# Performance work log

Hardware: AMD Instinct MI355X
Metric: run time of the kernel (lower is better)

Reference implementation:

```python
import jax, jax.numpy as jnp
import numpy as np

NUM_ENT = 50000
NUM_REL = 64
NUM_TRI = 400000
DIN = 128
DOUT = 128
DREL = 128
NUM_HEAD = 8
DH = DOUT // NUM_HEAD


def setup_inputs() -> dict:
    key = jax.random.key(0)
    ks = jax.random.split(key, 9)
    emb_ent = jax.random.normal(ks[0], (NUM_ENT, DIN), jnp.float32)
    emb_rel = jax.random.normal(ks[1], (NUM_REL, DREL), jnp.float32)
    heads = jax.random.randint(ks[2], (NUM_TRI,), 0, NUM_ENT)
    rels = jax.random.randint(ks[3], (NUM_TRI,), 0, NUM_REL)
    tails = jax.random.randint(ks[4], (NUM_TRI,), 0, NUM_ENT)
    triplets = jnp.stack([heads, rels, tails], axis=-1)
    # xavier-normal-like init (stored as [in, out]; torch Linear applies x @ W.T)
    Wa = jax.random.normal(ks[5], (2 * DIN + DREL, DOUT), jnp.float32) * (2.0 / (2 * DIN + DREL + DOUT)) ** 0.5
    ba = jnp.zeros((DOUT,), jnp.float32)
    attn_vec = jax.random.normal(ks[6], (1, NUM_HEAD, DH), jnp.float32) * 0.1
    Wg = jax.random.normal(ks[7], (DIN + DREL, DOUT), jnp.float32) * (2.0 / (DIN + DREL + DOUT)) ** 0.5
    bg = jnp.zeros((DOUT,), jnp.float32)
    return {"emb_ent": emb_ent, "emb_rel": emb_rel, "triplets": triplets,
            "Wa": Wa, "ba": ba, "attn_vec": attn_vec, "Wg": Wg, "bg": bg}


def reference(emb_ent, emb_rel, triplets, Wa, ba, attn_vec, Wg, bg):
    num_ent = emb_ent.shape[0]
    n_head, d_hid = attn_vec.shape[1], attn_vec.shape[2]
    head, rel, tail = triplets[:, 0], triplets[:, 1], triplets[:, 2]

    # in-degree of each entity (as attention-softmax denominator for self_rel)
    ent_freq = jax.ops.segment_sum(jnp.ones(tail.shape, jnp.float32), tail,
                                   num_segments=num_ent)[:, None]
    # torch adds 1e-16 to all entries iff any entry is zero
    ent_freq = ent_freq + jnp.where(jnp.any(ent_freq == 0.0), 1e-16, 0.0)

    # mean relation embedding of incoming edges per entity -> self-loop relation
    self_rel = jax.ops.segment_sum(emb_rel[rel], tail, num_segments=num_ent) / ent_freq

    # append self-loops: one per entity
    emb_rels = jnp.concatenate([emb_rel[rel], self_rel], axis=0)       # [E+N, dr]
    ar = jnp.arange(num_ent)
    head_all = jnp.concatenate([head, ar], axis=0)                     # [E+N]
    tail_all = jnp.concatenate([tail, ar], axis=0)                     # [E+N]

    # attention logits per edge per head
    feat_att = jnp.concatenate([emb_ent[tail_all], emb_ent[head_all], emb_rels], axis=-1)
    h = jnp.tanh(feat_att @ Wa + ba).reshape(-1, n_head, d_hid)
    attn_raw = jnp.sum(h * attn_vec, axis=-1, keepdims=True)           # [E+N, H, 1]

    # segment softmax over edges sharing a tail (every segment has a self-loop)
    amax = jax.ops.segment_max(attn_raw, tail_all, num_segments=num_ent)
    attn_val = jnp.exp(attn_raw - amax[tail_all])
    asum = jax.ops.segment_sum(attn_val, tail_all, num_segments=num_ent)
    beta = attn_val / (asum[tail_all] + 1e-16)                         # [E+N, H, 1]

    # message projection and weighted aggregation
    msg = (jnp.concatenate([emb_ent[head_all], emb_rels], axis=-1) @ Wg + bg)
    msg = msg.reshape(-1, n_head, d_hid)
    out = jax.ops.segment_sum(beta * msg, tail_all, num_segments=num_ent)
    return out.reshape(num_ent, -1)
```

## Files before the change

### kernel.cpp

```cpp
#include <hip/hip_runtime.h>
#include <math.h>

#define NUM_ENT  50000
#define NUM_REL  64
#define NUM_TRI  400000
#define DIN      128
#define CAP      64

#define PACK_BLOCKS  24
#define SMALL_BLOCKS 64
#define ZERO_BLOCKS  196
#define PREP_BLOCKS  (PACK_BLOCKS + SMALL_BLOCKS + ZERO_BLOCKS)

#define ENT_BLOCKS   782
#define SCAT_BLOCKS  391
#define MID_BLOCKS   (ENT_BLOCKS + SCAT_BLOCKS)

typedef __attribute__((ext_vector_type(8))) short bf16x8;
typedef __attribute__((ext_vector_type(4))) float f32x4;

__device__ __forceinline__ float4 f4add(float4 a, float4 b) {
    return make_float4(a.x + b.x, a.y + b.y, a.z + b.z, a.w + b.w);
}

__device__ __forceinline__ unsigned short f2bf(float f) {
    unsigned u = __float_as_uint(f);
    unsigned r = ((u >> 16) & 1u) + 0x7fffu;
    return (unsigned short)((u + r) >> 16);
}
__device__ __forceinline__ float bf2f(unsigned short h) {
    return __uint_as_float(((unsigned)h) << 16);
}
__device__ __forceinline__ float4 ldbf4(const unsigned short* p) {
    ushort4 u = *(const ushort4*)p;
    return make_float4(bf2f(u.x), bf2f(u.y), bf2f(u.z), bf2f(u.w));
}
__device__ __forceinline__ void ldbf8(const unsigned short* p, float4* lo, float4* hi) {
    ushort4 u0 = *(const ushort4*)p;
    ushort4 u1 = *(const ushort4*)(p + 4);
    *lo = make_float4(bf2f(u0.x), bf2f(u0.y), bf2f(u0.z), bf2f(u0.w));
    *hi = make_float4(bf2f(u1.x), bf2f(u1.y), bf2f(u1.z), bf2f(u1.w));
}

__device__ __forceinline__ float tanhf_fast(float x) {
    float e = __expf(2.f * x);
    return 1.f - 2.f * __builtin_amdgcn_rcpf(e + 1.f);
}
__device__ __forceinline__ float tanh_dot4(float4 x, float4 av) {
    return tanhf_fast(x.x) * av.x + tanhf_fast(x.y) * av.y +
           tanhf_fast(x.z) * av.z + tanhf_fast(x.w) * av.w;
}

__global__ __launch_bounds__(256) void k_prep(const float* __restrict__ emb_rel,
                                              const float* __restrict__ Wa,
                                              const float* __restrict__ Wg,
                                              unsigned short* __restrict__ Bpack,
                                              unsigned short* __restrict__ TaTg,
                                              int* __restrict__ deg) {
    __shared__ float s[DIN];
    int b = blockIdx.x;
    int tid = threadIdx.x;

    if (b < PACK_BLOCKS) {
        for (int i = 0; i < 8; i++) {
            int idx = b * 2048 + i * 256 + tid;
            int j    = idx & 7;
            int lane = (idx >> 3) & 63;
            int ks   = (idx >> 9) & 3;
            int t    = (idx >> 11) & 7;
            int w    = idx >> 14;
            int k = ks * 32 + ((lane >> 4) << 3) + j;
            int n = t * 16 + (lane & 15);
            const float* W = (w == 0) ? Wa : (w == 1) ? (Wa + 128 * DIN) : Wg;
            Bpack[idx] = f2bf(W[k * DIN + n]);
        }
    } else if (b < PACK_BLOCKS + SMALL_BLOCKS) {
        int row = b - PACK_BLOCKS;
        if (tid < DIN) s[tid] = emb_rel[row * DIN + tid];
        __syncthreads();
        int j = tid & 127;
        const float* W = (tid < 128) ? (Wa + 256 * DIN) : (Wg + 128 * DIN);
        float acc = 0.f;
#pragma unroll 8
        for (int k = 0; k < DIN; k++) acc += s[k] * W[k * DIN + j];
        int pos = row * 256 + 8 * (j >> 2) + (j & 3) + ((tid < 128) ? 0 : 4);
        TaTg[pos] = f2bf(acc);
    } else {
        int idx = (b - PACK_BLOCKS - SMALL_BLOCKS) * 256 + tid;
        if (idx < NUM_ENT) deg[idx] = 0;
    }
}

__global__ __launch_bounds__(256) void k_mid(const float* __restrict__ X,
                                             const unsigned short* __restrict__ Bpack,
                                             const int* __restrict__ trip,
                                             const float* __restrict__ ba,
                                             const float* __restrict__ bg,
                                             unsigned short* __restrict__ Pt,
                                             unsigned short* __restrict__ PhGh,
                                             int* __restrict__ deg,
                                             int* __restrict__ elist) {
    __shared__ unsigned short As[64][136];
    int b = blockIdx.x;
    int tid = threadIdx.x;

    if (b < ENT_BLOCKS) {
        int m0 = b * 64;
        for (int i = 0; i < 8; i++) {
            int v = tid + i * 256;
            int row = v >> 5;
            int c4 = v & 31;
            int gr = m0 + row;
            if (gr >= NUM_ENT) gr = NUM_ENT - 1;
            float4 x = *(const float4*)&X[gr * DIN + c4 * 4];
            ushort4 h;
            h.x = f2bf(x.x); h.y = f2bf(x.y); h.z = f2bf(x.z); h.w = f2bf(x.w);
            *(ushort4*)&As[row][c4 * 4] = h;
        }
        __syncthreads();

        int w = tid >> 6;
        int q = tid & 63;
        int quad = q >> 4;
        int lrow = w * 16 + (q & 15);
        int gr = m0 + lrow;

        bf16x8 a[4];
#pragma unroll
        for (int ks = 0; ks < 4; ks++)
            a[ks] = *(const bf16x8*)&As[lrow][ks * 32 + quad * 8];

        const bf16x8* Bp = (const bf16x8*)Bpack;
#pragma unroll
        for (int s = 0; s < 3; s++) {
            f32x4 acc[8];
#pragma unroll
            for (int t = 0; t < 8; t++) acc[t] = (f32x4){0.f, 0.f, 0.f, 0.f};
#pragma unroll
            for (int ks = 0; ks < 4; ks++) {
#pragma unroll
                for (int t = 0; t < 8; t++) {
                    bf16x8 wf = Bp[((s * 8 + t) * 4 + ks) * 64 + q];
                    acc[t] = __builtin_amdgcn_mfma_f32_16x16x32_bf16(wf, a[ks], acc[t], 0, 0, 0);
                }
            }
            if (gr < NUM_ENT) {
#pragma unroll
                for (int t = 0; t < 8; t++) {
                    int n0 = t * 16 + quad * 4;
                    float4 bb = make_float4(0.f, 0.f, 0.f, 0.f);
                    if (s == 0) bb = *(const float4*)&ba[n0];
                    if (s == 2) bb = *(const float4*)&bg[n0];
                    ushort4 o;
                    o.x = f2bf(acc[t][0] + bb.x);
                    o.y = f2bf(acc[t][1] + bb.y);
                    o.z = f2bf(acc[t][2] + bb.z);
                    o.w = f2bf(acc[t][3] + bb.w);
                    if (s == 0) {
                        *(ushort4*)&Pt[gr * DIN + n0] = o;
                    } else {
                        *(ushort4*)&PhGh[gr * 256 + 2 * n0 + ((s == 1) ? 0 : 4)] = o;
                    }
                }
            }
        }
    } else {
        int i0 = (b - ENT_BLOCKS) * 1024 + tid * 4;
        if (i0 < NUM_TRI) {
            const int4* tp = (const int4*)&trip[i0 * 3];
            int4 A = tp[0], B4 = tp[1], C4 = tp[2];
            int hs[4] = {A.x, A.w, B4.z, C4.y};
            int rs[4] = {A.y, B4.x, B4.w, C4.z};
            int ts[4] = {A.z, B4.y, C4.x, C4.w};
#pragma unroll
            for (int u = 0; u < 4; u++) {
                int pos = atomicAdd(&deg[ts[u]], 1);
                if (pos < CAP) elist[ts[u] * CAP + pos] = (hs[u] << 6) | rs[u];
            }
        }
    }
}

__global__ __launch_bounds__(256) void k_fused(const int* __restrict__ elist,
                                               const int* __restrict__ deg_arr,
                                               const unsigned short* __restrict__ Pt,
                                               const unsigned short* __restrict__ PhGh,
                                               const unsigned short* __restrict__ TaTg,
                                               const float* __restrict__ attn_vec,
                                               float* __restrict__ out) {
    int tid = threadIdx.x;
    int wv = tid >> 6;
    int lane = tid & 63;
    int half = lane >> 5;
    int q = lane & 31;
    int t = blockIdx.x * 4 + wv;
    int deg = deg_arr[t];
    if (deg > CAP) deg = CAP;
    int c = q * 4;

    float4 pt4 = ldbf4(&Pt[t * DIN + c]);
    float4 av4 = *(const float4*)&attn_vec[c];

    int eall = elist[t * CAP + lane];

    float l = 0.f;
    float4 acc = make_float4(0.f, 0.f, 0.f, 0.f);
    float4 sTa = make_float4(0.f, 0.f, 0.f, 0.f);
    float4 sTg = make_float4(0.f, 0.f, 0.f, 0.f);

    for (int it = half; it < deg; it += 2) {
        int e = __shfl(eall, it);
        int h = e >> 6;
        int r = e & 63;
        float4 ta, tg, ph, gh;
        ldbf8(&TaTg[r * 256 + q * 8], &ta, &tg);
        ldbf8(&PhGh[h * 256 + q * 8], &ph, &gh);
        sTa = f4add(sTa, ta);
        sTg = f4add(sTg, tg);
        float4 pa = f4add(ph, ta);
        float4 gm = f4add(gh, tg);
        float p = tanh_dot4(f4add(pt4, pa), av4);
        p += __shfl_xor(p, 1);
        p += __shfl_xor(p, 2);
        float w = __expf(p);
        l += w;
        acc.x += w * gm.x; acc.y += w * gm.y; acc.z += w * gm.z; acc.w += w * gm.w;
    }

    l     += __shfl_xor(l, 32);
    acc.x += __shfl_xor(acc.x, 32);
    acc.y += __shfl_xor(acc.y, 32);
    acc.z += __shfl_xor(acc.z, 32);
    acc.w += __shfl_xor(acc.w, 32);
    sTa.x += __shfl_xor(sTa.x, 32);
    sTa.y += __shfl_xor(sTa.y, 32);
    sTa.z += __shfl_xor(sTa.z, 32);
    sTa.w += __shfl_xor(sTa.w, 32);
    sTg.x += __shfl_xor(sTg.x, 32);
    sTg.y += __shfl_xor(sTg.y, 32);
    sTg.z += __shfl_xor(sTg.z, 32);
    sTg.w += __shfl_xor(sTg.w, 32);

    {
        float inv = (deg > 0) ? __builtin_amdgcn_rcpf((float)deg) : 0.f;
        float4 pa, gm;
        ldbf8(&PhGh[t * 256 + q * 8], &pa, &gm);
        pa.x += sTa.x * inv; pa.y += sTa.y * inv; pa.z += sTa.z * inv; pa.w += sTa.w * inv;
        gm.x += sTg.x * inv; gm.y += sTg.y * inv; gm.z += sTg.z * inv; gm.w += sTg.w * inv;
        float p = tanh_dot4(f4add(pt4, pa), av4);
        p += __shfl_xor(p, 1);
        p += __shfl_xor(p, 2);
        float w = __expf(p);
        l += w;
        acc.x += w * gm.x; acc.y += w * gm.y; acc.z += w * gm.z; acc.w += w * gm.w;
    }
    float invl = 1.f / (l + 1e-16f);
    if (half == 0) {
        *(float4*)&out[t * DIN + c] =
            make_float4(acc.x * invl, acc.y * invl, acc.z * invl, acc.w * invl);
    }
}

extern "C" void kernel_launch(void* const* d_in, const int* in_sizes, int n_in,
                              void* d_out, int out_size, void* d_ws, size_t ws_size,
                              hipStream_t stream) {
    const float* emb_ent  = (const float*)d_in[0];
    const float* emb_rel  = (const float*)d_in[1];
    const int*   trip     = (const int*)d_in[2];
    const float* Wa       = (const float*)d_in[3];
    const float* ba       = (const float*)d_in[4];
    const float* attn_vec = (const float*)d_in[5];
    const float* Wg       = (const float*)d_in[6];
    const float* bg       = (const float*)d_in[7];
    float* out = (float*)d_out;

    unsigned short* wsh = (unsigned short*)d_ws;
    unsigned short* Pt    = wsh;
    unsigned short* PhGh  = wsh + 6400000;
    unsigned short* TaTg  = wsh + 19200000;
    unsigned short* Bpack = wsh + 19216384;
    int* deg   = (int*)(wsh + 19265536);
    int* elist = deg + 50000;

    k_prep<<<PREP_BLOCKS, 256, 0, stream>>>(emb_rel, Wa, Wg, Bpack, TaTg, deg);

    k_mid<<<MID_BLOCKS, 256, 0, stream>>>(emb_ent, Bpack, trip, ba, bg,
                                          Pt, PhGh, deg, elist);

    k_fused<<<NUM_ENT / 4, 256, 0, stream>>>(elist, deg,
                                             Pt, PhGh, TaTg, attn_vec, out);
}
```

Before: 189.8 us.

## Split mid kernel into scatter and GEMM kernels, unroll edge loop by two

Splits the combined GEMM and edge-scatter kernel into two separate launches, k_scat and k_gemm, so each has a uniform block workload. The per-entity edge loop in k_fused now handles two edges per iteration so the gathers for both are in flight together, with a tail step for the remaining edge. ldbf8 now uses a single 16-byte vector load instead of two 8-byte loads. This costs one extra kernel launch and the overlap between scatter atomics and GEMM blocks that one launch allowed.

New measurement: 185.5 us. 1.02x faster.

```diff
diff --git a/kernel.cpp b/kernel.cpp
--- a/kernel.cpp
+++ b/kernel.cpp
@@ -14,9 +14,9 @@
 
 #define ENT_BLOCKS   782
 #define SCAT_BLOCKS  391
-#define MID_BLOCKS   (ENT_BLOCKS + SCAT_BLOCKS)
 
 typedef __attribute__((ext_vector_type(8))) short bf16x8;
+typedef __attribute__((ext_vector_type(8))) unsigned short u16x8;
 typedef __attribute__((ext_vector_type(4))) float f32x4;
 
 __device__ __forceinline__ float4 f4add(float4 a, float4 b) {
@@ -36,10 +36,9 @@
     return make_float4(bf2f(u.x), bf2f(u.y), bf2f(u.z), bf2f(u.w));
 }
 __device__ __forceinline__ void ldbf8(const unsigned short* p, float4* lo, float4* hi) {
-    ushort4 u0 = *(const ushort4*)p;
-    ushort4 u1 = *(const ushort4*)(p + 4);
-    *lo = make_float4(bf2f(u0.x), bf2f(u0.y), bf2f(u0.z), bf2f(u0.w));
-    *hi = make_float4(bf2f(u1.x), bf2f(u1.y), bf2f(u1.z), bf2f(u1.w));
+    u16x8 u = *(const u16x8*)p;
+    *lo = make_float4(bf2f(u[0]), bf2f(u[1]), bf2f(u[2]), bf2f(u[3]));
+    *hi = make_float4(bf2f(u[4]), bf2f(u[5]), bf2f(u[6]), bf2f(u[7]));
 }
 
 __device__ __forceinline__ float tanhf_fast(float x) {
@@ -91,91 +90,92 @@
     }
 }
 
-__global__ __launch_bounds__(256) void k_mid(const float* __restrict__ X,
-                                             const unsigned short* __restrict__ Bpack,
-                                             const int* __restrict__ trip,
-                                             const float* __restrict__ ba,
-                                             const float* __restrict__ bg,
-                                             unsigned short* __restrict__ Pt,
-                                             unsigned short* __restrict__ PhGh,
-                                             int* __restrict__ deg,
-                                             int* __restrict__ elist) {
+__global__ __launch_bounds__(256) void k_scat(const int* __restrict__ trip,
+                                              int* __restrict__ deg,
+                                              int* __restrict__ elist) {
+    int b = blockIdx.x;
+    int tid = threadIdx.x;
+    int i0 = b * 1024 + tid * 4;
+    if (i0 < NUM_TRI) {
+        const int4* tp = (const int4*)&trip[i0 * 3];
+        int4 A = tp[0], B4 = tp[1], C4 = tp[2];
+        int hs[4] = {A.x, A.w, B4.z, C4.y};
+        int rs[4] = {A.y, B4.x, B4.w, C4.z};
+        int ts[4] = {A.z, B4.y, C4.x, C4.w};
+#pragma unroll
+        for (int u = 0; u < 4; u++) {
+            int pos = atomicAdd(&deg[ts[u]], 1);
+            if (pos < CAP) elist[ts[u] * CAP + pos] = (hs[u] << 6) | rs[u];
+        }
+    }
+}
+
+__global__ __launch_bounds__(256) void k_gemm(const float* __restrict__ X,
+                                              const unsigned short* __restrict__ Bpack,
+                                              const float* __restrict__ ba,
+                                              const float* __restrict__ bg,
+                                              unsigned short* __restrict__ Pt,
+                                              unsigned short* __restrict__ PhGh) {
     __shared__ unsigned short As[64][136];
     int b = blockIdx.x;
     int tid = threadIdx.x;
 
-    if (b < ENT_BLOCKS) {
-        int m0 = b * 64;
-        for (int i = 0; i < 8; i++) {
-            int v = tid + i * 256;
-            int row = v >> 5;
-            int c4 = v & 31;
-            int gr = m0 + row;
-            if (gr >= NUM_ENT) gr = NUM_ENT - 1;
-            float4 x = *(const float4*)&X[gr * DIN + c4 * 4];
-            ushort4 h;
-            h.x = f2bf(x.x); h.y = f2bf(x.y); h.z = f2bf(x.z); h.w = f2bf(x.w);
-            *(ushort4*)&As[row][c4 * 4] = h;
-        }
-        __syncthreads();
-
-        int w = tid >> 6;
-        int q = tid & 63;
-        int quad = q >> 4;
-        int lrow = w * 16 + (q & 15);
-        int gr = m0 + lrow;
-
-        bf16x8 a[4];
-#pragma unroll
-        for (int ks = 0; ks < 4; ks++)
-            a[ks] = *(const bf16x8*)&As[lrow][ks * 32 + quad * 8];
-
-        const bf16x8* Bp = (const bf16x8*)Bpack;
-#pragma unroll
-        for (int s = 0; s < 3; s++) {
-            f32x4 acc[8];
-#pragma unroll
-            for (int t = 0; t < 8; t++) acc[t] = (f32x4){0.f, 0.f, 0.f, 0.f};
-#pragma unroll
-            for (int ks = 0; ks < 4; ks++) {
-#pragma unroll
-                for (int t = 0; t < 8; t++) {
-                    bf16x8 wf = Bp[((s * 8 + t) * 4 + ks) * 64 + q];
-                    acc[t] = __builtin_amdgcn_mfma_f32_16x16x32_bf16(wf, a[ks], acc[t], 0, 0, 0);
+    int m0 = b * 64;
+    for (int i = 0; i < 8; i++) {
+        int v = tid + i * 256;
+        int row = v >> 5;
+        int c4 = v & 31;
+        int gr = m0 + row;
+        if (gr >= NUM_ENT) gr = NUM_ENT - 1;
+        float4 x = *(const float4*)&X[gr * DIN + c4 * 4];
+        ushort4 h;
+        h.x = f2bf(x.x); h.y = f2bf(x.y); h.z = f2bf(x.z); h.w = f2bf(x.w);
+        *(ushort4*)&As[row][c4 * 4] = h;
+    }
+    __syncthreads();
+
+    int w = tid >> 6;
+    int q = tid & 63;
+    int quad = q >> 4;
+    int lrow = w * 16 + (q & 15);
+    int gr = m0 + lrow;
+
+    bf16x8 a[4];
+#pragma unroll
+    for (int ks = 0; ks < 4; ks++)
+        a[ks] = *(const bf16x8*)&As[lrow][ks * 32 + quad * 8];
+
+    const bf16x8* Bp = (const bf16x8*)Bpack;
+#pragma unroll
+    for (int s = 0; s < 3; s++) {
+        f32x4 acc[8];
+#pragma unroll
+        for (int t = 0; t < 8; t++) acc[t] = (f32x4){0.f, 0.f, 0.f, 0.f};
+#pragma unroll
+        for (int ks = 0; ks < 4; ks++) {
+#pragma unroll
+            for (int t = 0; t < 8; t++) {
+                bf16x8 wf = Bp[((s * 8 + t) * 4 + ks) * 64 + q];
+                acc[t] = __builtin_amdgcn_mfma_f32_16x16x32_bf16(wf, a[ks], acc[t], 0, 0, 0);
+            }
+        }
+        if (gr < NUM_ENT) {
+#pragma unroll
+            for (int t = 0; t < 8; t++) {
+                int n0 = t * 16 + quad * 4;
+                float4 bb = make_float4(0.f, 0.f, 0.f, 0.f);
+                if (s == 0) bb = *(const float4*)&ba[n0];
+                if (s == 2) bb = *(const float4*)&bg[n0];
+                ushort4 o;
+                o.x = f2bf(acc[t][0] + bb.x);
+                o.y = f2bf(acc[t][1] + bb.y);
+                o.z = f2bf(acc[t][2] + bb.z);
+                o.w = f2bf(acc[t][3] + bb.w);
+                if (s == 0) {
+                    *(ushort4*)&Pt[gr * DIN + n0] = o;
+                } else {
+                    *(ushort4*)&PhGh[gr * 256 + 2 * n0 + ((s == 1) ? 0 : 4)] = o;
                 }
-            }
-            if (gr < NUM_ENT) {
-#pragma unroll
-                for (int t = 0; t < 8; t++) {
-                    int n0 = t * 16 + quad * 4;
-                    float4 bb = make_float4(0.f, 0.f, 0.f, 0.f);
-                    if (s == 0) bb = *(const float4*)&ba[n0];
-                    if (s == 2) bb = *(const float4*)&bg[n0];
-                    ushort4 o;
-                    o.x = f2bf(acc[t][0] + bb.x);
-                    o.y = f2bf(acc[t][1] + bb.y);
-                    o.z = f2bf(acc[t][2] + bb.z);
-                    o.w = f2bf(acc[t][3] + bb.w);
-                    if (s == 0) {
-                        *(ushort4*)&Pt[gr * DIN + n0] = o;
-                    } else {
-                        *(ushort4*)&PhGh[gr * 256 + 2 * n0 + ((s == 1) ? 0 : 4)] = o;
-                    }
-                }
-            }
-        }
-    } else {
-        int i0 = (b - ENT_BLOCKS) * 1024 + tid * 4;
-        if (i0 < NUM_TRI) {
-            const int4* tp = (const int4*)&trip[i0 * 3];
-            int4 A = tp[0], B4 = tp[1], C4 = tp[2];
-            int hs[4] = {A.x, A.w, B4.z, C4.y};
-            int rs[4] = {A.y, B4.x, B4.w, C4.z};
-            int ts[4] = {A.z, B4.y, C4.x, C4.w};
-#pragma unroll
-            for (int u = 0; u < 4; u++) {
-                int pos = atomicAdd(&deg[ts[u]], 1);
-                if (pos < CAP) elist[ts[u] * CAP + pos] = (hs[u] << 6) | rs[u];
             }
         }
     }
@@ -208,23 +208,57 @@
     float4 sTa = make_float4(0.f, 0.f, 0.f, 0.f);
     float4 sTg = make_float4(0.f, 0.f, 0.f, 0.f);
 
-    for (int it = half; it < deg; it += 2) {
-        int e = __shfl(eall, it);
-        int h = e >> 6;
-        int r = e & 63;
-        float4 ta, tg, ph, gh;
-        ldbf8(&TaTg[r * 256 + q * 8], &ta, &tg);
-        ldbf8(&PhGh[h * 256 + q * 8], &ph, &gh);
-        sTa = f4add(sTa, ta);
-        sTg = f4add(sTg, tg);
-        float4 pa = f4add(ph, ta);
-        float4 gm = f4add(gh, tg);
-        float p = tanh_dot4(f4add(pt4, pa), av4);
-        p += __shfl_xor(p, 1);
-        p += __shfl_xor(p, 2);
-        float w = __expf(p);
-        l += w;
-        acc.x += w * gm.x; acc.y += w * gm.y; acc.z += w * gm.z; acc.w += w * gm.w;
+    int it = half;
+    for (; it + 2 < deg; it += 4) {
+        int e0 = __shfl(eall, it);
+        int e1 = __shfl(eall, it + 2);
+        int h0 = e0 >> 6, r0 = e0 & 63;
+        int h1 = e1 >> 6, r1 = e1 & 63;
+        float4 ta0, tg0, ph0, gh0, ta1, tg1, ph1, gh1;
+        ldbf8(&TaTg[r0 * 256 + q * 8], &ta0, &tg0);
+        ldbf8(&PhGh[h0 * 256 + q * 8], &ph0, &gh0);
+        ldbf8(&TaTg[r1 * 256 + q * 8], &ta1, &tg1);
+        ldbf8(&PhGh[h1 * 256 + q * 8], &ph1, &gh1);
+
+        sTa = f4add(sTa, f4add(ta0, ta1));
+        sTg = f4add(sTg, f4add(tg0, tg1));
+        float4 pa0 = f4add(ph0, ta0);
+        float4 gm0 = f4add(gh0, tg0);
+        float4 pa1 = f4add(ph1, ta1);
+        float4 gm1 = f4add(gh1, tg1);
+        float p0 = tanh_dot4(f4add(pt4, pa0), av4);
+        float p1 = tanh_dot4(f4add(pt4, pa1), av4);
+        p0 += __shfl_xor(p0, 1);
+        p0 += __shfl_xor(p0, 2);
+        p1 += __shfl_xor(p1, 1);
+        p1 += __shfl_xor(p1, 2);
+        float w0 = __expf(p0);
+        float w1 = __expf(p1);
+        l += w0 + w1;
+        acc.x += w0 * gm0.x + w1 * gm1.x;
+        acc.y += w0 * gm0.y + w1 * gm1.y;
+        acc.z += w0 * gm0.z + w1 * gm1.z;
+        acc.w += w0 * gm0.w + w1 * gm1.w;
+    }
+    {
+        int e = __shfl(eall, it & (CAP - 1));
+        if (it < deg) {
+            int h = e >> 6;
+            int r = e & 63;
+            float4 ta, tg, ph, gh;
+            ldbf8(&TaTg[r * 256 + q * 8], &ta, &tg);
+            ldbf8(&PhGh[h * 256 + q * 8], &ph, &gh);
+            sTa = f4add(sTa, ta);
+            sTg = f4add(sTg, tg);
+            float4 pa = f4add(ph, ta);
+            float4 gm = f4add(gh, tg);
+            float p = tanh_dot4(f4add(pt4, pa), av4);
+            p += __shfl_xor(p, 1);
+            p += __shfl_xor(p, 2);
+            float w = __expf(p);
+            l += w;
+            acc.x += w * gm.x; acc.y += w * gm.y; acc.z += w * gm.z; acc.w += w * gm.w;
+        }
     }
 
     l     += __shfl_xor(l, 32);
@@ -284,8 +318,9 @@
 
     k_prep<<<PREP_BLOCKS, 256, 0, stream>>>(emb_rel, Wa, Wg, Bpack, TaTg, deg);
 
-    k_mid<<<MID_BLOCKS, 256, 0, stream>>>(emb_ent, Bpack, trip, ba, bg,
-                                          Pt, PhGh, deg, elist);
+    k_scat<<<SCAT_BLOCKS, 256, 0, stream>>>(trip, deg, elist);
+
+    k_gemm<<<ENT_BLOCKS, 256, 0, stream>>>(emb_ent, Bpack, ba, bg, Pt, PhGh);
 
     k_fused<<<NUM_ENT / 4, 256, 0, stream>>>(elist, deg,
                                              Pt, PhGh, TaTg, attn_vec, out);
```
